# Kernel tuning notes

Measured on AMD Instinct MI355X. Metric: run time of the kernel, lower is better.

The kernel has to match this reference:

```python
import jax, jax.numpy as jnp
import numpy as np

EPS = 1e-06
NUM_HEADS = 16
THETA = 10000.0


def rope_tables(grid_size, head_dim):
    # matches VisionRotaryEmbeddingFast: 2D rope, table shape [grid^2, head_dim]
    half = head_dim // 2
    freqs = 1.0 / THETA ** (jnp.arange(0, half, 2, dtype=jnp.float32) / half)
    freqs = jnp.concatenate([freqs, freqs], axis=0)  # [half]
    t = jnp.arange(grid_size, dtype=jnp.float32)
    f = jnp.outer(t, freqs)  # [grid, half]
    fh = jnp.broadcast_to(f[:, None, :], (grid_size, grid_size, half))
    fw = jnp.broadcast_to(f[None, :, :], (grid_size, grid_size, half))
    full = jnp.concatenate([fh, fw], axis=-1).reshape(-1, head_dim)  # [N, head_dim]
    return jnp.cos(full), jnp.sin(full)


def rotate_half(x):
    n = x.shape[-1] // 2
    return jnp.concatenate((-x[..., n:], x[..., :n]), axis=-1)


def rms_norm(x, gamma):
    var = jnp.mean(x * x, axis=-1, keepdims=True)
    return x * jax.lax.rsqrt(var + EPS) * gamma


def setup_inputs() -> dict:
    key = jax.random.key(0)
    ks = jax.random.split(key, 5)
    B, N, C = 32, 1024, 1024
    return {
        "x": jax.random.normal(ks[0], (B, N, C), dtype=jnp.float32),
        "qkv_w": jax.random.normal(ks[1], (C, 3 * C), dtype=jnp.float32) * (C ** -0.5),
        "qkv_b": jnp.zeros((3 * C,), dtype=jnp.float32),
        "proj_w": jax.random.normal(ks[2], (C, C), dtype=jnp.float32) * (C ** -0.5),
        "proj_b": jnp.zeros((C,), dtype=jnp.float32),
        "q_gamma": jnp.ones((C // NUM_HEADS,), dtype=jnp.float32),
        "k_gamma": jnp.ones((C // NUM_HEADS,), dtype=jnp.float32),
    }


def reference(x, qkv_w, qkv_b, proj_w, proj_b, q_gamma, k_gamma):
    B, N, C = x.shape
    H = NUM_HEADS
    hd = C // H
    grid = int(np.sqrt(N))
    cos, sin = rope_tables(grid, hd)  # [N, hd] each
    cos = cos[None, :, None, :]  # broadcast over [B, N, H, hd]
    sin = sin[None, :, None, :]

    qkv = (x @ qkv_w + qkv_b).reshape(B, N, 3, H, hd)
    q, k, v = qkv[:, :, 0], qkv[:, :, 1], qkv[:, :, 2]  # [B, N, H, hd]

    q = rms_norm(q, q_gamma)
    k = rms_norm(k, k_gamma)
    q = q * cos + rotate_half(q) * sin
    k = k * cos + rotate_half(k) * sin

    out = jax.nn.dot_product_attention(q, k, v, is_causal=False)  # [B, N, H, hd]
    out = out.reshape(B, N, C)
    return out @ proj_w + proj_b
```

## Files before the change

kernel.cpp:

```cpp
#include <hip/hip_runtime.h>
#include <stdint.h>

typedef float f32x4 __attribute__((ext_vector_type(4)));
typedef float f32x16 __attribute__((ext_vector_type(16)));
typedef short s16x8 __attribute__((ext_vector_type(8)));
typedef unsigned short u16;

__device__ __forceinline__ u16 f2bf(float f) {
  union { float f; uint32_t u; } c; c.f = f;
  uint32_t u = c.u;
  u = (u + 0x7fffu + ((u >> 16) & 1u)) >> 16;
  return (u16)u;
}

__device__ __forceinline__ void gload16(const void* g, void* lds) {
  __builtin_amdgcn_global_load_lds(
      (const __attribute__((address_space(1))) void*)g,
      (__attribute__((address_space(3))) void*)lds, 16, 0, 0);
}

__device__ __forceinline__ f32x4 mfma16(s16x8 a, s16x8 b, f32x4 c) {
  return __builtin_amdgcn_mfma_f32_16x16x32_bf16(a, b, c, 0, 0, 0);
}

__device__ __forceinline__ f32x16 mfma32(s16x8 a, s16x8 b, f32x16 c) {
  return __builtin_amdgcn_mfma_f32_32x32x16_bf16(a, b, c, 0, 0, 0);
}

__device__ __forceinline__ int swz(int row, int c8) {
  return row * 64 + ((c8 ^ (row & 7)) << 3);
}

__global__ void cvt_bf16(const float* __restrict__ in, u16* __restrict__ out, size_t n) {
  size_t i = ((size_t)blockIdx.x * blockDim.x + threadIdx.x) * 4;
  if (i < n) {
    float4 v = *(const float4*)&in[i];
    u16 o0 = f2bf(v.x), o1 = f2bf(v.y), o2 = f2bf(v.z), o3 = f2bf(v.w);
    uint2 packed;
    packed.x = (uint32_t)o0 | ((uint32_t)o1 << 16);
    packed.y = (uint32_t)o2 | ((uint32_t)o3 << 16);
    *(uint2*)&out[i] = packed;
  }
}

__global__ void transpose_cvt(const float* __restrict__ in, u16* __restrict__ out,
                              int rows, int cols) {
  __shared__ float tile[64][65];
  const int c0 = blockIdx.x * 64, r0 = blockIdx.y * 64;
  const int tr = threadIdx.x >> 6, tc = threadIdx.x & 63;
#pragma unroll
  for (int i = 0; i < 16; i++) {
    int r = i * 4 + tr;
    tile[r][tc] = in[(size_t)(r0 + r) * cols + c0 + tc];
  }
  __syncthreads();
#pragma unroll
  for (int i = 0; i < 16; i++) {
    int oc = i * 4 + tr;
    out[(size_t)(c0 + oc) * rows + r0 + tc] = f2bf(tile[tc][oc]);
  }
}

__global__ void rope_tables_kernel(float* __restrict__ cosT, float* __restrict__ sinT) {
  int n = blockIdx.x;
  int d = threadIdx.x;
  int ph = n >> 5, pw = n & 31;
  int pos = (d < 32) ? ph : pw;
  int fi = d & 15;
  float freq = powf(10000.f, -(float)fi / 16.f);
  float ang = (float)pos * freq;
  cosT[n * 64 + d] = cosf(ang);
  sinT[n * 64 + d] = sinf(ang);
}


#define PH_MID \
  __builtin_amdgcn_sched_barrier(0); \
  __builtin_amdgcn_s_barrier(); \
  asm volatile("s_waitcnt lgkmcnt(0)" ::: "memory"); \
  __builtin_amdgcn_sched_barrier(0); \
  __builtin_amdgcn_s_setprio(1);

#define PH_END \
  __builtin_amdgcn_s_setprio(0); \
  __builtin_amdgcn_sched_barrier(0); \
  __builtin_amdgcn_s_barrier(); \
  __builtin_amdgcn_sched_barrier(0);

#define STAGE(ldsoff, g) do { \
    gload16((g) + (size_t)(w8 + srow) * 1024 + sc8 * 8,       &lds[(ldsoff) + w8 * 64]); \
    gload16((g) + (size_t)(w8 + srow + 64) * 1024 + sc8 * 8,  &lds[(ldsoff) + (w8 + 64) * 64]); \
  } while (0)

#define RD_A(dst, BUF, mh) \
  _Pragma("unroll") \
  for (int mi = 0; mi < 4; mi++) { \
    dst[mi][0] = *(const s16x8*)&lds[(BUF) * 32768 + arow0 + ((mh) * 64 + mi * 16) * 64 + swz0]; \
    dst[mi][1] = *(const s16x8*)&lds[(BUF) * 32768 + arow0 + ((mh) * 64 + mi * 16) * 64 + swz1]; \
  }

#define RD_B(dst, BUF, nh) \
  _Pragma("unroll") \
  for (int ni = 0; ni < 2; ni++) { \
    dst[ni][0] = *(const s16x8*)&lds[(BUF) * 32768 + 16384 + brow0 + ((nh) * 32 + ni * 16) * 64 + swz0]; \
    dst[ni][1] = *(const s16x8*)&lds[(BUF) * 32768 + 16384 + brow0 + ((nh) * 32 + ni * 16) * 64 + swz1]; \
  }

#define MFMA_QUAD(af, bfr, mh, nh) \
  _Pragma("unroll") \
  for (int mi = 0; mi < 4; mi++) \
    _Pragma("unroll") \
    for (int ni = 0; ni < 2; ni++) { \
      acc[(mh) * 4 + mi][(nh) * 2 + ni] = mfma16(af[mi][0], bfr[ni][0], acc[(mh) * 4 + mi][(nh) * 2 + ni]); \
      acc[(mh) * 4 + mi][(nh) * 2 + ni] = mfma16(af[mi][1], bfr[ni][1], acc[(mh) * 4 + mi][(nh) * 2 + ni]); \
    }

#define KTILE(BUF, KT, MODE) do { \
    s16x8 a0f[4][2], a1f[4][2], b0f[2][2], b1f[2][2]; \
     \
    RD_A(a0f, BUF, 0); \
    RD_B(b0f, BUF, 0); \
    if ((MODE) < 2) STAGE((1 - (BUF)) * 32768, Ag + (size_t)((KT) + 1) * 64); \
    PH_MID; MFMA_QUAD(a0f, b0f, 0, 0); PH_END; \
     \
    RD_B(b1f, BUF, 1); \
    if ((MODE) < 2) STAGE((1 - (BUF)) * 32768 + 8192, Ag + (size_t)128 * 1024 + ((KT) + 1) * 64); \
    PH_MID; MFMA_QUAD(a0f, b1f, 0, 1); PH_END; \
     \
    RD_A(a1f, BUF, 1); \
    if ((MODE) == 0) STAGE((BUF) * 32768 + 16384, Bg + (size_t)((KT) + 2) * 64); \
    PH_MID; MFMA_QUAD(a1f, b1f, 1, 1); PH_END; \
     \
    if ((MODE) == 0) STAGE((BUF) * 32768 + 16384 + 8192, Bg + (size_t)128 * 1024 + ((KT) + 2) * 64); \
    PH_MID; MFMA_QUAD(a1f, b0f, 1, 0); \
    __builtin_amdgcn_s_setprio(0); \
    if ((MODE) == 0) asm volatile("s_waitcnt vmcnt(4)" ::: "memory"); \
    if ((MODE) == 1) asm volatile("s_waitcnt vmcnt(0)" ::: "memory"); \
    __builtin_amdgcn_sched_barrier(0); \
    __builtin_amdgcn_s_barrier(); \
    __builtin_amdgcn_sched_barrier(0); \
  } while (0)

__device__ __forceinline__ void gemm_mainloop_8ph(
    const u16* __restrict__ Ag, const u16* __restrict__ Bg,
    u16* lds, f32x4 (&acc)[8][4])
{
  const int t = threadIdx.x;
  const int l = t & 63, w = t >> 6;
  const int wm = w & 1, wn = w >> 1;
  const int lrow = l & 15, lg = l >> 4;
  const int srow = l >> 3, sc8 = (l & 7) ^ srow;
  const int w8 = w * 8;
  const int swz0 = ((0 + lg) ^ (lrow & 7)) << 3;
  const int swz1 = ((4 + lg) ^ (lrow & 7)) << 3;
  const int arow0 = (wm * 128 + lrow) * 64;
  const int brow0 = (wn * 64 + lrow) * 64;

  STAGE(0,                 Ag);
  STAGE(8192,              Ag + (size_t)128 * 1024);
  STAGE(16384,             Bg);
  STAGE(16384 + 8192,      Bg + (size_t)128 * 1024);
  STAGE(32768 + 16384,          Bg + 64);
  STAGE(32768 + 16384 + 8192,   Bg + (size_t)128 * 1024 + 64);
  asm volatile("s_waitcnt vmcnt(4)" ::: "memory");
  __builtin_amdgcn_sched_barrier(0);
  __builtin_amdgcn_s_barrier();
  __builtin_amdgcn_sched_barrier(0);

#pragma unroll 1
  for (int kt = 0; kt < 14; kt += 2) {
    KTILE(0, kt, 0);
    KTILE(1, kt + 1, 0);
  }
  KTILE(0, 14, 1);
  KTILE(1, 15, 2);
}

__global__ __launch_bounds__(512, 2) void gemm_qkv(
    const u16* __restrict__ A,
    const u16* __restrict__ Bt,
    const float* __restrict__ bias,
    const float* __restrict__ qgam, const float* __restrict__ kgam,
    const float* __restrict__ cosT, const float* __restrict__ sinT,
    u16* __restrict__ qb, u16* __restrict__ kb, u16* __restrict__ vb)
{
  __shared__ u16 lds[65536];
  const int bid = blockIdx.x;
  const int sb = (bid & 7) * 192 + (bid >> 3);
  const int bm = sb / 12, bn = sb % 12;

  const f32x4 fzero = {0.f, 0.f, 0.f, 0.f};
  f32x4 acc[8][4];
#pragma unroll
  for (int i = 0; i < 8; i++)
#pragma unroll
    for (int j = 0; j < 4; j++) acc[i][j] = fzero;

  gemm_mainloop_8ph(A + (size_t)bm * 256 * 1024, Bt + (size_t)bn * 256 * 1024, lds, acc);

  const int t = threadIdx.x, l = t & 63, w = t >> 6;
  const int wm = w & 1, wn = w >> 1, lrow = l & 15, lg = l >> 4;
  const int colb = bn * 256 + wn * 64;
  const int s = colb >> 10;
  const int h = (colb & 1023) >> 6;

  float biasv[4];
#pragma unroll
  for (int nt = 0; nt < 4; nt++) biasv[nt] = bias[colb + nt * 16 + lrow];

  if (s < 2) {
    u16* dst = (s == 0) ? qb : kb;
    const float mul = (s == 0) ? 0.18033688011112042f : 1.0f;
    const float* gamma = (s == 0) ? qgam : kgam;
    float g[4];
#pragma unroll
    for (int nt = 0; nt < 4; nt++) g[nt] = gamma[nt * 16 + lrow] * mul;
#pragma unroll
    for (int mf = 0; mf < 8; mf++) {
#pragma unroll
      for (int r = 0; r < 4; r++) {
        const int rowg = bm * 256 + wm * 128 + mf * 16 + lg * 4 + r;
        const int b = rowg >> 10, np = rowg & 1023;
        float tmp[4]; float sq = 0.f;
#pragma unroll
        for (int nt = 0; nt < 4; nt++) {
          float v = acc[mf][nt][r] + biasv[nt];
          tmp[nt] = v; sq += v * v;
        }
#pragma unroll
        for (int off = 1; off < 16; off <<= 1) sq += __shfl_xor(sq, off);
        const float rstd = rsqrtf(sq * 0.015625f + 1e-6f);
#pragma unroll
        for (int nt = 0; nt < 4; nt++) tmp[nt] *= rstd * g[nt];
        const size_t base = (((size_t)(b * 16 + h)) * 1024 + np) * 64;
#pragma unroll
        for (int nt = 0; nt < 4; nt++) {
          const int d = nt * 16 + lrow;
          const float cv = cosT[np * 64 + d], sv = sinT[np * 64 + d];
          const float rh = (nt < 2) ? -tmp[nt + 2] : tmp[nt - 2];
          dst[base + d] = f2bf(tmp[nt] * cv + rh * sv);
        }
      }
    }
  } else {
#pragma unroll
    for (int mf = 0; mf < 8; mf++) {
#pragma unroll
      for (int r = 0; r < 4; r++) {
        const int rowg = bm * 256 + wm * 128 + mf * 16 + lg * 4 + r;
        const int b = rowg >> 10, np = rowg & 1023;
        const size_t hb = ((size_t)(b * 16 + h)) * 64;
#pragma unroll
        for (int nt = 0; nt < 4; nt++) {
          const int d = nt * 16 + lrow;
          vb[(hb + d) * 1024 + np] = f2bf(acc[mf][nt][r] + biasv[nt]);
        }
      }
    }
  }
}

__global__ __launch_bounds__(256, 3) void attn_kernel(
    const u16* __restrict__ qbuf, const u16* __restrict__ kbuf,
    const u16* __restrict__ vtbuf, u16* __restrict__ obuf)
{
  __shared__ u16 Qs[128 * 64];
  __shared__ u16 Ks[2][64 * 64];
  __shared__ u16 VTs[2][64 * 64];
  __shared__ float lsumS[4][32];
  const int bx = blockIdx.x;
  const int bh = bx >> 3, qt = bx & 7;
  const int t = threadIdx.x, l = t & 63, w = t >> 6;
  const int q31 = l & 31, hi = l >> 5;

  const u16* qg  = qbuf  + (size_t)bh * 65536 + (size_t)qt * 8192;
  const u16* kg0 = kbuf  + (size_t)bh * 65536;
  const u16* vt0 = vtbuf + (size_t)bh * 65536;

  const int srow = l >> 3;
  const int sc8  = (l & 7) ^ (srow & 7);

#pragma unroll
  for (int i = 0; i < 4; i++) {
    const int r0 = (w + i * 4) * 8;
    gload16(qg + (size_t)(r0 + srow) * 64 + sc8 * 8, &Qs[r0 * 64]);
  }
#pragma unroll
  for (int i = 0; i < 2; i++) {
    const int r0 = (w + i * 4) * 8;
    gload16(kg0 + (size_t)(r0 + srow) * 64 + sc8 * 8, &Ks[0][r0 * 64]);
    gload16(vt0 + (size_t)(r0 + srow) * 1024 + sc8 * 8, &VTs[0][r0 * 64]);
  }
  asm volatile("s_waitcnt vmcnt(0)" ::: "memory");
  __syncthreads();

  s16x8 bq[4];
#pragma unroll
  for (int ds = 0; ds < 4; ds++)
    bq[ds] = *(const s16x8*)&Qs[swz(w * 32 + q31, ds * 2 + hi)];

  f32x16 o0, o1;
#pragma unroll
  for (int i = 0; i < 16; i++) { o0[i] = 0.f; o1[i] = 0.f; }
  float l_ = 0.f;

#pragma unroll 2
  for (int kt = 0; kt < 16; kt++) {
    const int cur = kt & 1;
    if (kt < 15) {
      const int kb = (kt + 1) * 64;
#pragma unroll
      for (int i = 0; i < 2; i++) {
        const int r0 = (w + i * 4) * 8;
        gload16(kg0 + (size_t)(kb + r0 + srow) * 64 + sc8 * 8, &Ks[cur ^ 1][r0 * 64]);
        gload16(vt0 + (size_t)(r0 + srow) * 1024 + kb + sc8 * 8, &VTs[cur ^ 1][r0 * 64]);
      }
    }

    f32x16 s0, s1;
#pragma unroll
    for (int i = 0; i < 16; i++) { s0[i] = 0.f; s1[i] = 0.f; }
    __builtin_amdgcn_s_setprio(1);
#pragma unroll
    for (int ds = 0; ds < 4; ds++) {
      s16x8 ak0 = *(const s16x8*)&Ks[cur][swz(q31, ds * 2 + hi)];
      s16x8 ak1 = *(const s16x8*)&Ks[cur][swz(32 + q31, ds * 2 + hi)];
      s0 = mfma32(ak0, bq[ds], s0);
      s1 = mfma32(ak1, bq[ds], s1);
    }
    __builtin_amdgcn_s_setprio(0);

    float p[32];
#pragma unroll
    for (int r = 0; r < 16; r++) p[r] = __builtin_amdgcn_exp2f(s0[r]);
#pragma unroll
    for (int r = 0; r < 16; r++) p[16 + r] = __builtin_amdgcn_exp2f(s1[r]);
    {
      float sm0 = 0.f, sm1 = 0.f, sm2 = 0.f, sm3 = 0.f;
#pragma unroll
      for (int r = 0; r < 8; r++) {
        sm0 += p[r]; sm1 += p[8 + r]; sm2 += p[16 + r]; sm3 += p[24 + r];
      }
      l_ += (sm0 + sm1) + (sm2 + sm3);
    }

    s16x8 pf[4];
#pragma unroll
    for (int j = 0; j < 4; j++) {
      uint32_t a1, b1, a2, b2;
      asm("v_cvt_pk_bf16_f32 %0, %1, %2" : "=v"(a1) : "v"(p[j * 8 + 0]), "v"(p[j * 8 + 1]));
      asm("v_cvt_pk_bf16_f32 %0, %1, %2" : "=v"(b1) : "v"(p[j * 8 + 2]), "v"(p[j * 8 + 3]));
      asm("v_cvt_pk_bf16_f32 %0, %1, %2" : "=v"(a2) : "v"(p[j * 8 + 4]), "v"(p[j * 8 + 5]));
      asm("v_cvt_pk_bf16_f32 %0, %1, %2" : "=v"(b2) : "v"(p[j * 8 + 6]), "v"(p[j * 8 + 7]));
      asm("v_permlane32_swap_b32 %0, %1" : "+v"(a1), "+v"(a2));
      asm("v_permlane32_swap_b32 %0, %1" : "+v"(b1), "+v"(b2));
      union { s16x8 v; uint32_t u[4]; } cvt;
      cvt.u[0] = a1; cvt.u[1] = b1; cvt.u[2] = a2; cvt.u[3] = b2;
      pf[j] = cvt.v;
    }

    __builtin_amdgcn_s_setprio(1);
#pragma unroll
    for (int j = 0; j < 4; j++) {
      s16x8 bv0 = *(const s16x8*)&VTs[cur][swz(q31, j * 2 + hi)];
      s16x8 bv1 = *(const s16x8*)&VTs[cur][swz(32 + q31, j * 2 + hi)];
      o0 = mfma32(pf[j], bv0, o0);
      o1 = mfma32(pf[j], bv1, o1);
    }
    __builtin_amdgcn_s_setprio(0);

    __syncthreads();
  }

  l_ += __shfl_xor(l_, 32);
  if (l < 32) lsumS[w][q31] = 1.0f / l_;

  const int b = bh >> 4, h = bh & 15;
#pragma unroll
  for (int r = 0; r < 16; r++) {
    const int q = (r & 3) + 8 * (r >> 2) + 4 * hi;
    const float inv = lsumS[w][q];
    const int n = qt * 128 + w * 32 + q;
    const size_t base = (((size_t)b * 1024 + n) * 16 + h) * 64;
    obuf[base + q31]      = f2bf(o0[r] * inv);
    obuf[base + 32 + q31] = f2bf(o1[r] * inv);
  }
}

__global__ __launch_bounds__(512, 2) void gemm_proj(
    const u16* __restrict__ A,
    const u16* __restrict__ Bt,
    const float* __restrict__ bias,
    float* __restrict__ out)
{
  __shared__ u16 lds[65536];
  const int bid = blockIdx.x;
  const int sb = (bid & 7) * 64 + (bid >> 3);
  const int bm = sb >> 2, bn = sb & 3;

  const f32x4 fzero = {0.f, 0.f, 0.f, 0.f};
  f32x4 acc[8][4];
#pragma unroll
  for (int i = 0; i < 8; i++)
#pragma unroll
    for (int j = 0; j < 4; j++) acc[i][j] = fzero;

  gemm_mainloop_8ph(A + (size_t)bm * 256 * 1024, Bt + (size_t)bn * 256 * 1024, lds, acc);

  const int t = threadIdx.x, l = t & 63, w = t >> 6;
  const int wm = w & 1, wn = w >> 1, lrow = l & 15, lg = l >> 4;
  const int colb = bn * 256 + wn * 64;
  float biasv[4];
#pragma unroll
  for (int nt = 0; nt < 4; nt++) biasv[nt] = bias[colb + nt * 16 + lrow];

#pragma unroll
  for (int mf = 0; mf < 8; mf++) {
#pragma unroll
    for (int r = 0; r < 4; r++) {
      const int rowg = bm * 256 + wm * 128 + mf * 16 + lg * 4 + r;
#pragma unroll
      for (int nt = 0; nt < 4; nt++) {
        const int col = colb + nt * 16 + lrow;
        out[(size_t)rowg * 1024 + col] = acc[mf][nt][r] + biasv[nt];
      }
    }
  }
}

extern "C" void kernel_launch(void* const* d_in, const int* in_sizes, int n_in,
                              void* d_out, int out_size, void* d_ws, size_t ws_size,
                              hipStream_t stream) {
  const float* x      = (const float*)d_in[0];
  const float* qkv_w  = (const float*)d_in[1];
  const float* qkv_b  = (const float*)d_in[2];
  const float* proj_w = (const float*)d_in[3];
  const float* proj_b = (const float*)d_in[4];
  const float* q_gam  = (const float*)d_in[5];
  const float* k_gam  = (const float*)d_in[6];

  char* ws = (char*)d_ws;
  u16*   xb   = (u16*)(ws);
  u16*   qb   = (u16*)(ws + 67108864);
  u16*   kb   = (u16*)(ws + 134217728);
  u16*   vb   = (u16*)(ws + 201326592);
  u16*   wqT  = (u16*)(ws + 268435456);
  u16*   wpT  = (u16*)(ws + 274726912);
  float* cosT = (float*)(ws + 276824064);
  float* sinT = (float*)(ws + 277086208);
  u16*   attn = xb;

  cvt_bf16<<<32768, 256, 0, stream>>>(x, xb, (size_t)33554432);
  transpose_cvt<<<dim3(48, 16), 256, 0, stream>>>(qkv_w, wqT, 1024, 3072);
  transpose_cvt<<<dim3(16, 16), 256, 0, stream>>>(proj_w, wpT, 1024, 1024);
  rope_tables_kernel<<<1024, 64, 0, stream>>>(cosT, sinT);

  gemm_qkv<<<dim3(1536), dim3(512), 0, stream>>>(xb, wqT, qkv_b, q_gam, k_gam,
                                                 cosT, sinT, qb, kb, vb);
  attn_kernel<<<4096, 256, 0, stream>>>(qb, kb, vb, attn);
  gemm_proj<<<dim3(512), dim3(512), 0, stream>>>(attn, wpT, proj_b, (float*)d_out);
}
```

Baseline: 713.6 us.

## Double attention query tile per block to reuse K/V across two query subtiles

Each attention block now processes 256 query rows instead of 128, with every wave handling two 32-row query subtiles. Each K and V^T tile loaded into shared memory therefore serves twice as many queries, halving total K/V global and LDS traffic and the number of blocks launched. The cost is roughly double the accumulator and score registers per wave, so the occupancy hint drops from 3 to 2 blocks per CU, and the grid shrinks to 2048 blocks.

```diff
diff --git a/kernel.cpp b/kernel.cpp
--- a/kernel.cpp
+++ b/kernel.cpp
@@ -260,20 +260,20 @@
   }
 }
 
-__global__ __launch_bounds__(256, 3) void attn_kernel(
+__global__ __launch_bounds__(256, 2) void attn_kernel(
     const u16* __restrict__ qbuf, const u16* __restrict__ kbuf,
     const u16* __restrict__ vtbuf, u16* __restrict__ obuf)
 {
-  __shared__ u16 Qs[128 * 64];
+  __shared__ u16 Qs[256 * 64];
   __shared__ u16 Ks[2][64 * 64];
   __shared__ u16 VTs[2][64 * 64];
-  __shared__ float lsumS[4][32];
+  __shared__ float lsumS[4][2][32];
   const int bx = blockIdx.x;
-  const int bh = bx >> 3, qt = bx & 7;
+  const int bh = bx >> 2, qt = bx & 3;
   const int t = threadIdx.x, l = t & 63, w = t >> 6;
   const int q31 = l & 31, hi = l >> 5;
 
-  const u16* qg  = qbuf  + (size_t)bh * 65536 + (size_t)qt * 8192;
+  const u16* qg  = qbuf  + (size_t)bh * 65536 + (size_t)qt * 16384;
   const u16* kg0 = kbuf  + (size_t)bh * 65536;
   const u16* vt0 = vtbuf + (size_t)bh * 65536;
 
@@ -281,7 +281,7 @@
   const int sc8  = (l & 7) ^ (srow & 7);
 
 #pragma unroll
-  for (int i = 0; i < 4; i++) {
+  for (int i = 0; i < 8; i++) {
     const int r0 = (w + i * 4) * 8;
     gload16(qg + (size_t)(r0 + srow) * 64 + sc8 * 8, &Qs[r0 * 64]);
   }
@@ -294,15 +294,21 @@
   asm volatile("s_waitcnt vmcnt(0)" ::: "memory");
   __syncthreads();
 
-  s16x8 bq[4];
-#pragma unroll
-  for (int ds = 0; ds < 4; ds++)
-    bq[ds] = *(const s16x8*)&Qs[swz(w * 32 + q31, ds * 2 + hi)];
-
-  f32x16 o0, o1;
-#pragma unroll
-  for (int i = 0; i < 16; i++) { o0[i] = 0.f; o1[i] = 0.f; }
-  float l_ = 0.f;
+  s16x8 bq[2][4];
+#pragma unroll
+  for (int qb = 0; qb < 2; qb++)
+#pragma unroll
+    for (int ds = 0; ds < 4; ds++)
+      bq[qb][ds] = *(const s16x8*)&Qs[swz(w * 64 + qb * 32 + q31, ds * 2 + hi)];
+
+  f32x16 o[2][2];
+#pragma unroll
+  for (int qb = 0; qb < 2; qb++)
+#pragma unroll
+    for (int kb2 = 0; kb2 < 2; kb2++)
+#pragma unroll
+      for (int i = 0; i < 16; i++) o[qb][kb2][i] = 0.f;
+  float l_[2] = {0.f, 0.f};
 
 #pragma unroll 2
   for (int kt = 0; kt < 16; kt++) {
@@ -317,46 +323,54 @@
       }
     }
 
-    f32x16 s0, s1;
-#pragma unroll
-    for (int i = 0; i < 16; i++) { s0[i] = 0.f; s1[i] = 0.f; }
+    f32x16 s[2][2];
+#pragma unroll
+    for (int qb = 0; qb < 2; qb++)
+#pragma unroll
+      for (int kb2 = 0; kb2 < 2; kb2++)
+#pragma unroll
+        for (int i = 0; i < 16; i++) s[qb][kb2][i] = 0.f;
     __builtin_amdgcn_s_setprio(1);
 #pragma unroll
     for (int ds = 0; ds < 4; ds++) {
       s16x8 ak0 = *(const s16x8*)&Ks[cur][swz(q31, ds * 2 + hi)];
       s16x8 ak1 = *(const s16x8*)&Ks[cur][swz(32 + q31, ds * 2 + hi)];
-      s0 = mfma32(ak0, bq[ds], s0);
-      s1 = mfma32(ak1, bq[ds], s1);
+      s[0][0] = mfma32(ak0, bq[0][ds], s[0][0]);
+      s[0][1] = mfma32(ak1, bq[0][ds], s[0][1]);
+      s[1][0] = mfma32(ak0, bq[1][ds], s[1][0]);
+      s[1][1] = mfma32(ak1, bq[1][ds], s[1][1]);
     }
     __builtin_amdgcn_s_setprio(0);
 
-    float p[32];
-#pragma unroll
-    for (int r = 0; r < 16; r++) p[r] = __builtin_amdgcn_exp2f(s0[r]);
-#pragma unroll
-    for (int r = 0; r < 16; r++) p[16 + r] = __builtin_amdgcn_exp2f(s1[r]);
-    {
-      float sm0 = 0.f, sm1 = 0.f, sm2 = 0.f, sm3 = 0.f;
-#pragma unroll
-      for (int r = 0; r < 8; r++) {
-        sm0 += p[r]; sm1 += p[8 + r]; sm2 += p[16 + r]; sm3 += p[24 + r];
-      }
-      l_ += (sm0 + sm1) + (sm2 + sm3);
-    }
-
-    s16x8 pf[4];
-#pragma unroll
-    for (int j = 0; j < 4; j++) {
-      uint32_t a1, b1, a2, b2;
-      asm("v_cvt_pk_bf16_f32 %0, %1, %2" : "=v"(a1) : "v"(p[j * 8 + 0]), "v"(p[j * 8 + 1]));
-      asm("v_cvt_pk_bf16_f32 %0, %1, %2" : "=v"(b1) : "v"(p[j * 8 + 2]), "v"(p[j * 8 + 3]));
-      asm("v_cvt_pk_bf16_f32 %0, %1, %2" : "=v"(a2) : "v"(p[j * 8 + 4]), "v"(p[j * 8 + 5]));
-      asm("v_cvt_pk_bf16_f32 %0, %1, %2" : "=v"(b2) : "v"(p[j * 8 + 6]), "v"(p[j * 8 + 7]));
-      asm("v_permlane32_swap_b32 %0, %1" : "+v"(a1), "+v"(a2));
-      asm("v_permlane32_swap_b32 %0, %1" : "+v"(b1), "+v"(b2));
-      union { s16x8 v; uint32_t u[4]; } cvt;
-      cvt.u[0] = a1; cvt.u[1] = b1; cvt.u[2] = a2; cvt.u[3] = b2;
-      pf[j] = cvt.v;
+    s16x8 pf[2][4];
+#pragma unroll
+    for (int qb = 0; qb < 2; qb++) {
+      float p[32];
+#pragma unroll
+      for (int r = 0; r < 16; r++) p[r] = __builtin_amdgcn_exp2f(s[qb][0][r]);
+#pragma unroll
+      for (int r = 0; r < 16; r++) p[16 + r] = __builtin_amdgcn_exp2f(s[qb][1][r]);
+      {
+        float sm0 = 0.f, sm1 = 0.f, sm2 = 0.f, sm3 = 0.f;
+#pragma unroll
+        for (int r = 0; r < 8; r++) {
+          sm0 += p[r]; sm1 += p[8 + r]; sm2 += p[16 + r]; sm3 += p[24 + r];
+        }
+        l_[qb] += (sm0 + sm1) + (sm2 + sm3);
+      }
+#pragma unroll
+      for (int j = 0; j < 4; j++) {
+        uint32_t a1, b1, a2, b2;
+        asm("v_cvt_pk_bf16_f32 %0, %1, %2" : "=v"(a1) : "v"(p[j * 8 + 0]), "v"(p[j * 8 + 1]));
+        asm("v_cvt_pk_bf16_f32 %0, %1, %2" : "=v"(b1) : "v"(p[j * 8 + 2]), "v"(p[j * 8 + 3]));
+        asm("v_cvt_pk_bf16_f32 %0, %1, %2" : "=v"(a2) : "v"(p[j * 8 + 4]), "v"(p[j * 8 + 5]));
+        asm("v_cvt_pk_bf16_f32 %0, %1, %2" : "=v"(b2) : "v"(p[j * 8 + 6]), "v"(p[j * 8 + 7]));
+        asm("v_permlane32_swap_b32 %0, %1" : "+v"(a1), "+v"(a2));
+        asm("v_permlane32_swap_b32 %0, %1" : "+v"(b1), "+v"(b2));
+        union { s16x8 v; uint32_t u[4]; } cvt;
+        cvt.u[0] = a1; cvt.u[1] = b1; cvt.u[2] = a2; cvt.u[3] = b2;
+        pf[qb][j] = cvt.v;
+      }
     }
 
     __builtin_amdgcn_s_setprio(1);
@@ -364,27 +378,34 @@
     for (int j = 0; j < 4; j++) {
       s16x8 bv0 = *(const s16x8*)&VTs[cur][swz(q31, j * 2 + hi)];
       s16x8 bv1 = *(const s16x8*)&VTs[cur][swz(32 + q31, j * 2 + hi)];
-      o0 = mfma32(pf[j], bv0, o0);
-      o1 = mfma32(pf[j], bv1, o1);
+      o[0][0] = mfma32(pf[0][j], bv0, o[0][0]);
+      o[0][1] = mfma32(pf[0][j], bv1, o[0][1]);
+      o[1][0] = mfma32(pf[1][j], bv0, o[1][0]);
+      o[1][1] = mfma32(pf[1][j], bv1, o[1][1]);
     }
     __builtin_amdgcn_s_setprio(0);
 
     __syncthreads();
   }
 
-  l_ += __shfl_xor(l_, 32);
-  if (l < 32) lsumS[w][q31] = 1.0f / l_;
+#pragma unroll
+  for (int qb = 0; qb < 2; qb++) {
+    l_[qb] += __shfl_xor(l_[qb], 32);
+    if (l < 32) lsumS[w][qb][q31] = 1.0f / l_[qb];
+  }
 
   const int b = bh >> 4, h = bh & 15;
 #pragma unroll
-  for (int r = 0; r < 16; r++) {
-    const int q = (r & 3) + 8 * (r >> 2) + 4 * hi;
-    const float inv = lsumS[w][q];
-    const int n = qt * 128 + w * 32 + q;
-    const size_t base = (((size_t)b * 1024 + n) * 16 + h) * 64;
-    obuf[base + q31]      = f2bf(o0[r] * inv);
-    obuf[base + 32 + q31] = f2bf(o1[r] * inv);
-  }
+  for (int qb = 0; qb < 2; qb++)
+#pragma unroll
+    for (int r = 0; r < 16; r++) {
+      const int q = (r & 3) + 8 * (r >> 2) + 4 * hi;
+      const float inv = lsumS[w][qb][q];
+      const int n = qt * 256 + w * 64 + qb * 32 + q;
+      const size_t base = (((size_t)b * 1024 + n) * 16 + h) * 64;
+      obuf[base + q31]      = f2bf(o[qb][0][r] * inv);
+      obuf[base + 32 + q31] = f2bf(o[qb][1][r] * inv);
+    }
 }
 
 __global__ __launch_bounds__(512, 2) void gemm_proj(
@@ -457,6 +478,6 @@
 
   gemm_qkv<<<dim3(1536), dim3(512), 0, stream>>>(xb, wqT, qkv_b, q_gam, k_gam,
                                                  cosT, sinT, qb, kb, vb);
-  attn_kernel<<<4096, 256, 0, stream>>>(qb, kb, vb, attn);
+  attn_kernel<<<2048, 256, 0, stream>>>(qb, kb, vb, attn);
   gemm_proj<<<dim3(512), dim3(512), 0, stream>>>(attn, wpT, proj_b, (float*)d_out);
 }
```

After: 691.1 us. 1.03x faster.
